# Optimization experiments

Measured on AMD Instinct MI355X. Metric: run time of the kernel, lower is better.

## Reference

```python
import jax, jax.numpy as jnp
import numpy as np

N_NODES = 100000
N_EDGES = 3200000
IN_DIM, HID_DIM, OUT_DIM = 128, 64, 2


def setup_inputs() -> dict:
    key = jax.random.key(0)
    k1, k2, k3, k4 = jax.random.split(key, 4)
    x = jax.random.normal(k1, (N_NODES, IN_DIM), dtype=jnp.float32)
    edge_index = jax.random.randint(k2, (2, N_EDGES), 0, N_NODES, dtype=jnp.int64)
    # GCNConv weights (glorot-style scale) and zero biases
    W1 = jax.random.normal(k3, (IN_DIM, HID_DIM), dtype=jnp.float32) / np.sqrt(IN_DIM)
    b1 = jnp.zeros((HID_DIM,), dtype=jnp.float32)
    W2 = jax.random.normal(k4, (HID_DIM, OUT_DIM), dtype=jnp.float32) / np.sqrt(HID_DIM)
    b2 = jnp.zeros((OUT_DIM,), dtype=jnp.float32)
    return {"x": x, "edge_index": edge_index, "W1": W1, "b1": b1, "W2": W2, "b2": b2}


def _gcn_norm(edge_index, num_nodes):
    # PyG GCNConv default: add self-loops, symmetric normalization deg^-1/2.
    loops = jnp.arange(num_nodes, dtype=edge_index.dtype)
    src = jnp.concatenate([edge_index[0], loops])  # [E+N]
    dst = jnp.concatenate([edge_index[1], loops])  # [E+N]
    deg = jax.ops.segment_sum(jnp.ones_like(dst, dtype=jnp.float32), dst,
                              num_segments=num_nodes)  # in-degree incl. self-loop
    dinv = jnp.where(deg > 0, jax.lax.rsqrt(deg), 0.0)
    norm = dinv[src] * dinv[dst]  # [E+N]
    return src, dst, norm


def _gcn_conv(h, W, b, src, dst, norm, num_nodes):
    h = h @ W                              # dense transform first (smaller dim)
    msg = h[src] * norm[:, None]           # gather + scale: [E+N, d]
    out = jax.ops.segment_sum(msg, dst, num_segments=num_nodes)  # scatter-add
    return out + b


def reference(x, edge_index, W1, b1, W2, b2):
    n = x.shape[0]
    src, dst, norm = _gcn_norm(edge_index, n)
    h = _gcn_conv(x, W1, b1, src, dst, norm, n)
    h = jax.nn.relu(h)
    return _gcn_conv(h, W2, b2, src, dst, norm, n)
```

## Files before the change

### kernel.cpp

```cpp
#include <hip/hip_runtime.h>
#include <hip/hip_bf16.h>


#define N_NODES 100000
#define IN_DIM 128
#define HID_DIM 64
#define OUT_DIM 2
#define NB 391
#define BCAP 12288
#define CHUNK 8192

typedef short bf16x8 __attribute__((ext_vector_type(8)));
typedef float f32x4 __attribute__((ext_vector_type(4)));

__device__ __forceinline__ unsigned short f2bf(float x) {
    unsigned int u = __float_as_uint(x);
    unsigned int r = (u + 0x7FFFu + ((u >> 16) & 1u)) >> 16;
    return (unsigned short)r;
}
__device__ __forceinline__ float bflo(unsigned int u) { return __uint_as_float(u << 16); }
__device__ __forceinline__ float bfhi(unsigned int u) { return __uint_as_float(u & 0xFFFF0000u); }
__device__ __forceinline__ int wave_incl_scan(int v, int laneid) {
#pragma unroll
    for (int off = 1; off < 64; off <<= 1) {
        int u = __shfl_up(v, off);
        if (laneid >= off) v += u;
    }
    return v;
}

__global__ __launch_bounds__(512) void part_kernel(const int* __restrict__ ei,
                                                   int* __restrict__ gCursor,
                                                   int* __restrict__ part, int E) {
    __shared__ int hist[512], lrow[512], gbase[512], lcur[512];
    __shared__ int lpk[CHUNK];
    __shared__ short lbkt[CHUNK];
    __shared__ int wsum[8], wofs[8];
    const int t = threadIdx.x;
    const int lane = t & 63, wv = t >> 6;
    const int base = blockIdx.x * CHUNK;
    const int cntC = min(CHUNK, E - base);

    hist[t] = 0;
    __syncthreads();

    int s[16], d[16];
    bool val[16];
    if (base + CHUNK <= E) {
#pragma unroll
        for (int i = 0; i < 4; ++i) {
            int4 sv = ((const int4*)(ei + base))[t + i * 512];
            int4 dv = ((const int4*)(ei + E + base))[t + i * 512];
            s[i * 4 + 0] = sv.x; s[i * 4 + 1] = sv.y; s[i * 4 + 2] = sv.z; s[i * 4 + 3] = sv.w;
            d[i * 4 + 0] = dv.x; d[i * 4 + 1] = dv.y; d[i * 4 + 2] = dv.z; d[i * 4 + 3] = dv.w;
            val[i * 4 + 0] = val[i * 4 + 1] = val[i * 4 + 2] = val[i * 4 + 3] = true;
        }
    } else {
#pragma unroll
        for (int i = 0; i < 16; ++i) {
            int e = base + t + i * 512;
            val[i] = (e < E);
            if (val[i]) {
                s[i] = ei[e];
                d[i] = ei[E + e];
            }
        }
    }
#pragma unroll
    for (int i = 0; i < 16; ++i)
        if (val[i]) atomicAdd(&hist[d[i] >> 8], 1);
    __syncthreads();

    int v = hist[t];
    int inc = wave_incl_scan(v, lane);
    if (lane == 63) wsum[wv] = inc;
    __syncthreads();
    if (t < 64) {
        int w = (t < 8) ? wsum[t] : 0;
        int wi = wave_incl_scan(w, t);
        if (t < 8) wofs[t] = wi - w;
    }
    __syncthreads();
    int excl = inc - v + wofs[wv];
    if (t < NB && v > 0) {
        int old = atomicAdd(&gCursor[t], v);
        gbase[t] = t * BCAP + old;
    }
    lcur[t] = excl;
    lrow[t] = excl;
    __syncthreads();

#pragma unroll
    for (int i = 0; i < 16; ++i) {
        if (val[i]) {
            int b = d[i] >> 8;
            int pos = atomicAdd(&lcur[b], 1);
            lpk[pos] = s[i] | ((d[i] & 255) << 20);
            lbkt[pos] = (short)b;
        }
    }
    __syncthreads();

    for (int i = t; i < cntC; i += 512) {
        int b = lbkt[i];
        int g = gbase[b] + (i - lrow[b]);
        if (g < (b + 1) * BCAP)
            part[g] = lpk[i];
    }
}

__global__ __launch_bounds__(1024) void csr_kernel(const int* __restrict__ part,
                                                   const int* __restrict__ gCursor,
                                                   int* __restrict__ cnt,
                                                   float* __restrict__ dinv,
                                                   int* __restrict__ rowptr,
                                                   int* __restrict__ csr_src, int n) {
    __shared__ int epk[BCAP];
    __shared__ int wcnt[16][256];
    __shared__ int wsum[4], wofs[4];
    const int b = blockIdx.x, t = threadIdx.x;
    const int lane = t & 63, wv = t >> 6;
    const int start = b * BCAP;
    const int count = min(gCursor[b], BCAP);

    for (int i = t; i < 16 * 256; i += 1024) ((int*)wcnt)[i] = 0;
    __syncthreads();
    for (int i = t; i < count; i += 1024) {
        int p = part[start + i];
        epk[i] = p;
        atomicAdd(&wcnt[wv][(p >> 20) & 255], 1);
    }
    __syncthreads();

    int v = 0;
    if (t < 256) {
        int sum = 0;
#pragma unroll
        for (int w = 0; w < 16; ++w) sum += wcnt[w][t];
        v = sum;
    }
    int inc = 0;
    if (t < 256) {
        inc = wave_incl_scan(v, lane);
        if (lane == 63) wsum[wv] = inc;
    }
    __syncthreads();
    if (t < 64) {
        int w = (t < 4) ? wsum[t] : 0;
        int wi = wave_incl_scan(w, t);
        if (t < 4) wofs[t] = wi - w;
    }
    __syncthreads();
    if (t < 256) {
        int excl = inc - v + wofs[wv];
        int node = (b << 8) + t;
        if (node < n) {
            cnt[node] = v;
            dinv[node] = rsqrtf((float)v + 1.0f);
            rowptr[node] = start + excl;
        }
        int run = excl;
#pragma unroll
        for (int w = 0; w < 16; ++w) {
            int c = wcnt[w][t];
            wcnt[w][t] = run;
            run += c;
        }
    }
    __syncthreads();

    for (int i = t; i < count; i += 1024) {
        int p = epk[i];
        int pos = atomicAdd(&wcnt[wv][(p >> 20) & 255], 1);
        csr_src[start + pos] = p & 0xFFFFF;
    }
}

__global__ __launch_bounds__(256) void gemm1_kernel(const float* __restrict__ x,
                                                    const float* __restrict__ W1,
                                                    const float* __restrict__ dinv,
                                                    unsigned short* __restrict__ hsb, int n) {
    __shared__ unsigned short sX[64 * 136];
    __shared__ unsigned short sW[64 * 136];
    const int tid = threadIdx.x;
    const int rbase = blockIdx.x * 64;

    for (int i = tid; i < 2048; i += 256) {
        int k = i >> 4, cq = (i & 15) << 2;
        float4 v = ((const float4*)W1)[i];
        sW[(cq + 0) * 136 + k] = f2bf(v.x);
        sW[(cq + 1) * 136 + k] = f2bf(v.y);
        sW[(cq + 2) * 136 + k] = f2bf(v.z);
        sW[(cq + 3) * 136 + k] = f2bf(v.w);
    }
    for (int i = tid; i < 2048; i += 256) {
        int r = i >> 5, kq = (i & 31) << 2;
        int gr = rbase + r;
        float4 v = make_float4(0.f, 0.f, 0.f, 0.f);
        if (gr < n) v = ((const float4*)x)[gr * 32 + (i & 31)];
        ushort4 u;
        u.x = f2bf(v.x); u.y = f2bf(v.y); u.z = f2bf(v.z); u.w = f2bf(v.w);
        *(ushort4*)&sX[r * 136 + kq] = u;
    }
    __syncthreads();

    const int wave = tid >> 6, lane = tid & 63;
    const int quad = lane >> 4, l16 = lane & 15;
    const int rowoff = wave * 16;

    f32x4 acc[4];
#pragma unroll
    for (int t = 0; t < 4; ++t) acc[t] = (f32x4){0.f, 0.f, 0.f, 0.f};

#pragma unroll
    for (int k0 = 0; k0 < 128; k0 += 32) {
        bf16x8 a = *(const bf16x8*)&sX[(rowoff + l16) * 136 + k0 + quad * 8];
#pragma unroll
        for (int t = 0; t < 4; ++t) {
            bf16x8 b = *(const bf16x8*)&sW[(t * 16 + l16) * 136 + k0 + quad * 8];
            acc[t] = __builtin_amdgcn_mfma_f32_16x16x32_bf16(a, b, acc[t], 0, 0, 0);
        }
    }

#pragma unroll
    for (int r = 0; r < 4; ++r) {
        int grow = rbase + rowoff + quad * 4 + r;
        if (grow < n) {
            float di = dinv[grow];
#pragma unroll
            for (int t = 0; t < 4; ++t)
                hsb[grow * HID_DIM + t * 16 + l16] = f2bf(acc[t][r] * di);
        }
    }
}

__global__ __launch_bounds__(256) void agg1_kernel(const int* __restrict__ rowptr,
                                                   const int* __restrict__ cnt,
                                                   const int* __restrict__ csr_src,
                                                   const unsigned short* __restrict__ hsb,
                                                   const float* __restrict__ dinv,
                                                   const float* __restrict__ b1,
                                                   const float* __restrict__ W2,
                                                   float* __restrict__ hs2, int n) {
    int node = blockIdx.x * 4 + (threadIdx.x >> 6);
    if (node >= n) return;
    int lane = threadIdx.x & 63;
    int g = lane >> 3;
    int l = lane & 7;
    int start = rowptr[node];
    int deg = cnt[node];

    float a[8] = {0.f, 0.f, 0.f, 0.f, 0.f, 0.f, 0.f, 0.f};
    int s0 = (g < deg)     ? csr_src[start + g]     : 0;
    int s1 = (g + 8 < deg) ? csr_src[start + g + 8] : 0;
    for (int j = g; j < deg; j += 16) {
        int p0 = (j + 16 < deg) ? csr_src[start + j + 16] : 0;
        int p1 = (j + 24 < deg) ? csr_src[start + j + 24] : 0;
        uint4 r0 = *(const uint4*)&hsb[(unsigned)s0 * HID_DIM + l * 8];
        uint4 r1 = *(const uint4*)&hsb[(unsigned)s1 * HID_DIM + l * 8];
        float m1 = (j + 8 < deg) ? 1.0f : 0.0f;
        a[0] += bflo(r0.x); a[1] += bfhi(r0.x);
        a[2] += bflo(r0.y); a[3] += bfhi(r0.y);
        a[4] += bflo(r0.z); a[5] += bfhi(r0.z);
        a[6] += bflo(r0.w); a[7] += bfhi(r0.w);
        a[0] = fmaf(m1, bflo(r1.x), a[0]); a[1] = fmaf(m1, bfhi(r1.x), a[1]);
        a[2] = fmaf(m1, bflo(r1.y), a[2]); a[3] = fmaf(m1, bfhi(r1.y), a[3]);
        a[4] = fmaf(m1, bflo(r1.z), a[4]); a[5] = fmaf(m1, bfhi(r1.z), a[5]);
        a[6] = fmaf(m1, bflo(r1.w), a[6]); a[7] = fmaf(m1, bfhi(r1.w), a[7]);
        s0 = p0; s1 = p1;
    }
#pragma unroll
    for (int off = 8; off <= 32; off <<= 1) {
#pragma unroll
        for (int i = 0; i < 8; ++i) a[i] += __shfl_xor(a[i], off);
    }

    {
        uint4 raw = *(const uint4*)&hsb[(unsigned)node * HID_DIM + l * 8];
        a[0] += bflo(raw.x); a[1] += bfhi(raw.x);
        a[2] += bflo(raw.y); a[3] += bfhi(raw.y);
        a[4] += bflo(raw.z); a[5] += bfhi(raw.z);
        a[6] += bflo(raw.w); a[7] += bfhi(raw.w);
    }

    float di = dinv[node];
    float4 bb0 = *(const float4*)&b1[l * 8];
    float4 bb1 = *(const float4*)&b1[l * 8 + 4];
    float t0 = fmaxf(fmaf(di, a[0], bb0.x), 0.0f);
    float t1 = fmaxf(fmaf(di, a[1], bb0.y), 0.0f);
    float t2 = fmaxf(fmaf(di, a[2], bb0.z), 0.0f);
    float t3 = fmaxf(fmaf(di, a[3], bb0.w), 0.0f);
    float t4 = fmaxf(fmaf(di, a[4], bb1.x), 0.0f);
    float t5 = fmaxf(fmaf(di, a[5], bb1.y), 0.0f);
    float t6 = fmaxf(fmaf(di, a[6], bb1.z), 0.0f);
    float t7 = fmaxf(fmaf(di, a[7], bb1.w), 0.0f);

    float4 w0 = *(const float4*)&W2[l * 16];
    float4 w1 = *(const float4*)&W2[l * 16 + 4];
    float4 w2 = *(const float4*)&W2[l * 16 + 8];
    float4 w3 = *(const float4*)&W2[l * 16 + 12];
    float p0 = t0 * w0.x + t1 * w0.z + t2 * w1.x + t3 * w1.z
             + t4 * w2.x + t5 * w2.z + t6 * w3.x + t7 * w3.z;
    float p1 = t0 * w0.y + t1 * w0.w + t2 * w1.y + t3 * w1.w
             + t4 * w2.y + t5 * w2.w + t6 * w3.y + t7 * w3.w;
    p0 += __shfl_xor(p0, 1);  p1 += __shfl_xor(p1, 1);
    p0 += __shfl_xor(p0, 2);  p1 += __shfl_xor(p1, 2);
    p0 += __shfl_xor(p0, 4);  p1 += __shfl_xor(p1, 4);

    if (lane == 0) {
        hs2[node * OUT_DIM + 0] = di * p0;
        hs2[node * OUT_DIM + 1] = di * p1;
    }
}

__global__ __launch_bounds__(256) void agg2_kernel(const int* __restrict__ rowptr,
                                                   const int* __restrict__ cnt,
                                                   const int* __restrict__ csr_src,
                                                   const float* __restrict__ hs2,
                                                   const float* __restrict__ dinv,
                                                   const float* __restrict__ b2,
                                                   float* __restrict__ out, int n) {
    int node = blockIdx.x * 4 + (threadIdx.x >> 6);
    if (node >= n) return;
    int lane = threadIdx.x & 63;
    int start = rowptr[node];
    int deg = cnt[node];

    float a0 = 0.0f, a1 = 0.0f;
    for (int j = lane; j < deg; j += 64) {
        int s = csr_src[start + j];
        float2 v = *(const float2*)&hs2[s * OUT_DIM];
        a0 += v.x;
        a1 += v.y;
    }
#pragma unroll
    for (int off = 32; off > 0; off >>= 1) {
        a0 += __shfl_xor(a0, off);
        a1 += __shfl_xor(a1, off);
    }
    if (lane == 0) {
        float di = dinv[node];
        float2 self = *(const float2*)&hs2[node * OUT_DIM];
        out[node * OUT_DIM + 0] = di * (a0 + self.x) + b2[0];
        out[node * OUT_DIM + 1] = di * (a1 + self.y) + b2[1];
    }
}

extern "C" void kernel_launch(void* const* d_in, const int* in_sizes, int n_in,
                              void* d_out, int out_size, void* d_ws, size_t ws_size,
                              hipStream_t stream) {
    const float* x  = (const float*)d_in[0];
    const int*   ei = (const int*)d_in[1];
    const float* W1 = (const float*)d_in[2];
    const float* b1 = (const float*)d_in[3];
    const float* W2 = (const float*)d_in[4];
    const float* b2 = (const float*)d_in[5];
    float* out = (float*)d_out;

    const int n = N_NODES;
    const int E = in_sizes[1] / 2;

    char* ws = (char*)d_ws;
    int*   gCursor = (int*)  (ws + 0);
    int*   cnt     = (int*)  (ws + (1u << 20));
    float* dinv    = (float*)(ws + (2u << 20));
    int*   rowptr  = (int*)  (ws + (3u << 20));
    float* hs2     = (float*)(ws + (4u << 20));
    int*   part    = (int*)  (ws + (5u << 20));
    unsigned short* hsb = (unsigned short*)(ws + (5u << 20));
    int*   csr_src = (int*)  (ws + (25u << 20));

    hipMemsetAsync(gCursor, 0, NB * sizeof(int), stream);

    part_kernel<<<(E + CHUNK - 1) / CHUNK, 512, 0, stream>>>(ei, gCursor, part, E);
    csr_kernel<<<NB, 1024, 0, stream>>>(part, gCursor, cnt, dinv, rowptr, csr_src, n);

    gemm1_kernel<<<(n + 63) / 64, 256, 0, stream>>>(x, W1, dinv, hsb, n);
    agg1_kernel<<<(n + 3) / 4, 256, 0, stream>>>(rowptr, cnt, csr_src, hsb, dinv, b1, W2, hs2, n);
    agg2_kernel<<<(n + 3) / 4, 256, 0, stream>>>(rowptr, cnt, csr_src, hs2, dinv, b2, out, n);
}
```

Baseline: 249.9 us.

## Keep CSR edges in registers, deepen agg1 gather unroll, half-wave agg2

The CSR build kernel now holds each thread's packed edges in a register array of CROUNDS entries instead of staging them in a shared-memory buffer, which frees LDS and may raise occupancy. The layer-1 aggregation processes four neighbor rows per iteration with prefetched indices, putting more gather loads in flight. Layer-2 aggregation assigns 32 lanes per node instead of 64, so fewer lanes sit idle given the average degree of about 32. Costs are more register pressure, and an implicit assumption that count never exceeds 12288, which holds because BCAP clamps it.

Measured after the change: 241.1 us. -3.5%, faster.

```diff
diff --git a/kernel.cpp b/kernel.cpp
--- a/kernel.cpp
+++ b/kernel.cpp
@@ -8,6 +8,7 @@
 #define OUT_DIM 2
 #define NB 391
 #define BCAP 12288
+#define CROUNDS 12
 #define CHUNK 8192
 
 typedef short bf16x8 __attribute__((ext_vector_type(8)));
@@ -20,6 +21,19 @@
 }
 __device__ __forceinline__ float bflo(unsigned int u) { return __uint_as_float(u << 16); }
 __device__ __forceinline__ float bfhi(unsigned int u) { return __uint_as_float(u & 0xFFFF0000u); }
+__device__ __forceinline__ float4 unplo(uint4 r) {
+    return make_float4(bflo(r.x), bflo(r.y), bflo(r.z), bflo(r.w));
+}
+__device__ __forceinline__ float4 unphi(uint4 r) {
+    return make_float4(bfhi(r.x), bfhi(r.y), bfhi(r.z), bfhi(r.w));
+}
+__device__ __forceinline__ float4 f4add(float4 a, float4 v) {
+    return make_float4(a.x + v.x, a.y + v.y, a.z + v.z, a.w + v.w);
+}
+__device__ __forceinline__ float4 f4fma(float m, float4 v, float4 a) {
+    return make_float4(fmaf(m, v.x, a.x), fmaf(m, v.y, a.y),
+                       fmaf(m, v.z, a.z), fmaf(m, v.w, a.w));
+}
 __device__ __forceinline__ int wave_incl_scan(int v, int laneid) {
 #pragma unroll
     for (int off = 1; off < 64; off <<= 1) {
@@ -115,7 +129,6 @@
                                                    float* __restrict__ dinv,
                                                    int* __restrict__ rowptr,
                                                    int* __restrict__ csr_src, int n) {
-    __shared__ int epk[BCAP];
     __shared__ int wcnt[16][256];
     __shared__ int wsum[4], wofs[4];
     const int b = blockIdx.x, t = threadIdx.x;
@@ -125,10 +138,15 @@
 
     for (int i = t; i < 16 * 256; i += 1024) ((int*)wcnt)[i] = 0;
     __syncthreads();
-    for (int i = t; i < count; i += 1024) {
-        int p = part[start + i];
-        epk[i] = p;
-        atomicAdd(&wcnt[wv][(p >> 20) & 255], 1);
+
+    int pk[CROUNDS];
+    bool val[CROUNDS];
+#pragma unroll
+    for (int k = 0; k < CROUNDS; ++k) {
+        int i = t + k * 1024;
+        val[k] = (i < count);
+        pk[k] = val[k] ? part[start + i] : 0;
+        if (val[k]) atomicAdd(&wcnt[wv][(pk[k] >> 20) & 255], 1);
     }
     __syncthreads();
 
@@ -169,10 +187,12 @@
     }
     __syncthreads();
 
-    for (int i = t; i < count; i += 1024) {
-        int p = epk[i];
-        int pos = atomicAdd(&wcnt[wv][(p >> 20) & 255], 1);
-        csr_src[start + pos] = p & 0xFFFFF;
+#pragma unroll
+    for (int k = 0; k < CROUNDS; ++k) {
+        if (val[k]) {
+            int pos = atomicAdd(&wcnt[wv][(pk[k] >> 20) & 255], 1);
+            csr_src[start + pos] = pk[k] & 0xFFFFF;
+        }
     }
 }
 
@@ -250,25 +270,35 @@
     int start = rowptr[node];
     int deg = cnt[node];
 
-    float a[8] = {0.f, 0.f, 0.f, 0.f, 0.f, 0.f, 0.f, 0.f};
-    int s0 = (g < deg)     ? csr_src[start + g]     : 0;
-    int s1 = (g + 8 < deg) ? csr_src[start + g + 8] : 0;
-    for (int j = g; j < deg; j += 16) {
-        int p0 = (j + 16 < deg) ? csr_src[start + j + 16] : 0;
-        int p1 = (j + 24 < deg) ? csr_src[start + j + 24] : 0;
+    float4 alo = make_float4(0.f, 0.f, 0.f, 0.f);
+    float4 ahi = make_float4(0.f, 0.f, 0.f, 0.f);
+    int s0 = (g      < deg) ? csr_src[start + g]      : 0;
+    int s1 = (g +  8 < deg) ? csr_src[start + g +  8] : 0;
+    int s2 = (g + 16 < deg) ? csr_src[start + g + 16] : 0;
+    int s3 = (g + 24 < deg) ? csr_src[start + g + 24] : 0;
+    for (int j = g; j < deg; j += 32) {
+        int p0 = (j + 32 < deg) ? csr_src[start + j + 32] : 0;
+        int p1 = (j + 40 < deg) ? csr_src[start + j + 40] : 0;
+        int p2 = (j + 48 < deg) ? csr_src[start + j + 48] : 0;
+        int p3 = (j + 56 < deg) ? csr_src[start + j + 56] : 0;
         uint4 r0 = *(const uint4*)&hsb[(unsigned)s0 * HID_DIM + l * 8];
         uint4 r1 = *(const uint4*)&hsb[(unsigned)s1 * HID_DIM + l * 8];
-        float m1 = (j + 8 < deg) ? 1.0f : 0.0f;
-        a[0] += bflo(r0.x); a[1] += bfhi(r0.x);
-        a[2] += bflo(r0.y); a[3] += bfhi(r0.y);
-        a[4] += bflo(r0.z); a[5] += bfhi(r0.z);
-        a[6] += bflo(r0.w); a[7] += bfhi(r0.w);
-        a[0] = fmaf(m1, bflo(r1.x), a[0]); a[1] = fmaf(m1, bfhi(r1.x), a[1]);
-        a[2] = fmaf(m1, bflo(r1.y), a[2]); a[3] = fmaf(m1, bfhi(r1.y), a[3]);
-        a[4] = fmaf(m1, bflo(r1.z), a[4]); a[5] = fmaf(m1, bfhi(r1.z), a[5]);
-        a[6] = fmaf(m1, bflo(r1.w), a[6]); a[7] = fmaf(m1, bfhi(r1.w), a[7]);
-        s0 = p0; s1 = p1;
-    }
+        uint4 r2 = *(const uint4*)&hsb[(unsigned)s2 * HID_DIM + l * 8];
+        uint4 r3 = *(const uint4*)&hsb[(unsigned)s3 * HID_DIM + l * 8];
+        float m1 = (j +  8 < deg) ? 1.0f : 0.0f;
+        float m2 = (j + 16 < deg) ? 1.0f : 0.0f;
+        float m3 = (j + 24 < deg) ? 1.0f : 0.0f;
+        alo = f4add(alo, unplo(r0));      ahi = f4add(ahi, unphi(r0));
+        alo = f4fma(m1, unplo(r1), alo);  ahi = f4fma(m1, unphi(r1), ahi);
+        alo = f4fma(m2, unplo(r2), alo);  ahi = f4fma(m2, unphi(r2), ahi);
+        alo = f4fma(m3, unplo(r3), alo);  ahi = f4fma(m3, unphi(r3), ahi);
+        s0 = p0; s1 = p1; s2 = p2; s3 = p3;
+    }
+
+    float a[8];
+    a[0] = alo.x; a[1] = ahi.x; a[2] = alo.y; a[3] = ahi.y;
+    a[4] = alo.z; a[5] = ahi.z; a[6] = alo.w; a[7] = ahi.w;
+
 #pragma unroll
     for (int off = 8; off <= 32; off <<= 1) {
 #pragma unroll
@@ -320,21 +350,21 @@
                                                    const float* __restrict__ dinv,
                                                    const float* __restrict__ b2,
                                                    float* __restrict__ out, int n) {
-    int node = blockIdx.x * 4 + (threadIdx.x >> 6);
+    int node = blockIdx.x * 8 + (threadIdx.x >> 5);
     if (node >= n) return;
-    int lane = threadIdx.x & 63;
+    int lane = threadIdx.x & 31;
     int start = rowptr[node];
     int deg = cnt[node];
 
     float a0 = 0.0f, a1 = 0.0f;
-    for (int j = lane; j < deg; j += 64) {
+    for (int j = lane; j < deg; j += 32) {
         int s = csr_src[start + j];
         float2 v = *(const float2*)&hs2[s * OUT_DIM];
         a0 += v.x;
         a1 += v.y;
     }
 #pragma unroll
-    for (int off = 32; off > 0; off >>= 1) {
+    for (int off = 16; off > 0; off >>= 1) {
         a0 += __shfl_xor(a0, off);
         a1 += __shfl_xor(a1, off);
     }
@@ -377,5 +407,5 @@
 
     gemm1_kernel<<<(n + 63) / 64, 256, 0, stream>>>(x, W1, dinv, hsb, n);
     agg1_kernel<<<(n + 3) / 4, 256, 0, stream>>>(rowptr, cnt, csr_src, hsb, dinv, b1, W2, hs2, n);
-    agg2_kernel<<<(n + 3) / 4, 256, 0, stream>>>(rowptr, cnt, csr_src, hs2, dinv, b2, out, n);
-}
+    agg2_kernel<<<(n + 7) / 8, 256, 0, stream>>>(rowptr, cnt, csr_src, hs2, dinv, b2, out, n);
+}
```
